# Kernel optimization log

Measured on AMD Instinct MI355X. Metric: run time of the kernel, lower is better.

The kernel has to match this reference:

```python
import jax, jax.numpy as jnp
import numpy as np

B, CIN, COUT, H, W = 8, 64, 128, 256, 256
BH = BW = 8          # block size
BC = 32              # block count per spatial dim
EPS = 1e-5


def _conv(x, w, b, pad):
    y = jax.lax.conv_general_dilated(
        x, w, (1, 1), [(pad, pad), (pad, pad)],
        dimension_numbers=("NCHW", "OIHW", "NCHW"))
    return y + b[None, :, None, None]


def _bn(x, g, b):
    # training-mode BatchNorm2d: per-channel batch stats over (N,H,W), biased var
    m = jnp.mean(x, axis=(0, 2, 3), keepdims=True)
    v = jnp.var(x, axis=(0, 2, 3), keepdims=True)
    return g[None, :, None, None] * (x - m) * jax.lax.rsqrt(v + EPS) + b[None, :, None, None]


def setup_inputs() -> dict:
    key = jax.random.key(0)
    ks = jax.random.split(key, 6)
    x = jax.random.normal(ks[0], (B, CIN, H, W), jnp.float32)
    ids = np.arange(0, B * BC * BC, 2)
    n = ids // (BC * BC)
    rem = ids % (BC * BC)
    abi = jnp.asarray(np.stack([n, rem // BC, rem % BC], axis=1), jnp.int32)

    def w(k, shape):
        return jax.random.normal(k, shape, jnp.float32) * 0.05

    C2 = 2 * COUT
    return dict(
        x=x, activeBlockIndices=abi,
        w_c=w(ks[1], (COUT, CIN, 1, 1)), b_c=jnp.zeros((COUT,), jnp.float32),
        g_c=jnp.ones((COUT,), jnp.float32), be_c=jnp.zeros((COUT,), jnp.float32),
        w1=w(ks[2], (C2, COUT, 1, 1)), b1=jnp.zeros((C2,), jnp.float32),
        g1=jnp.ones((C2,), jnp.float32), be1=jnp.zeros((C2,), jnp.float32),
        w2=w(ks[3], (C2, C2, 3, 3)), b2=jnp.zeros((C2,), jnp.float32),
        g2=jnp.ones((C2,), jnp.float32), be2=jnp.zeros((C2,), jnp.float32),
        w3=w(ks[4], (COUT, C2, 1, 1)), b3=jnp.zeros((COUT,), jnp.float32),
        g3=jnp.ones((COUT,), jnp.float32), be3=jnp.zeros((COUT,), jnp.float32),
    )


def reference(x, activeBlockIndices,
              w_c, b_c, g_c, be_c,
              w1, b1, g1, be1,
              w2, b2, g2, be2,
              w3, b3, g3, be3):
    # channel stack: 1x1 conv -> ReLU -> BN
    x = _bn(jax.nn.relu(_conv(x, w_c, b_c, 0)), g_c, be_c)  # [B, COUT, H, W]

    n = activeBlockIndices[:, 0]
    rows = activeBlockIndices[:, 1][:, None] * BH + jnp.arange(BH)  # [NB, BH]
    cols = activeBlockIndices[:, 2][:, None] * BW + jnp.arange(BW)  # [NB, BW]

    # sparse_gather: advanced indexing -> [NB, BH, BW, COUT]
    g = x[n[:, None, None], :, rows[:, :, None], cols[:, None, :]]
    g = g.transpose(0, 3, 1, 2)  # [NB, COUT, BH, BW]

    # dense stack on gathered blocks
    g = _bn(jax.nn.relu(_conv(g, w1, b1, 0)), g1, be1)
    g = _bn(jax.nn.relu(_conv(g, w2, b2, 1)), g2, be2)
    g = _bn(jax.nn.relu(_conv(g, w3, b3, 0)), g3, be3)  # [NB, COUT, BH, BW]

    # sparse_scatter back into x
    x = x.at[n[:, None, None], :, rows[:, :, None], cols[:, None, :]].set(
        g.transpose(0, 2, 3, 1))
    return x
```

## Files before the change

### kernel.cpp

```cpp
#include <hip/hip_runtime.h>
#include <hip/hip_bf16.h>
#include <stdint.h>

typedef unsigned short u16;

#define B_    8
#define CIN_  64
#define COUT_ 128
#define C2_   256
#define H_    256
#define W_    256
#define HW_   (H_*W_)
#define EPS_  1e-5f

typedef __attribute__((ext_vector_type(8))) short bf16x8;
typedef __attribute__((ext_vector_type(4))) float f32x4;

__device__ __align__(16) u16  g_R0[67108864];
__device__ __align__(16) u16  g_R1[67108864];
__device__ float g_wTa[8192];
__device__ float g_stat[4096];
__device__ __align__(16) u16 g_w2pk[1179648];
__device__ float g_S2[2304];
__device__ float g_bias2p[16384];
__device__ __align__(16) u16 g_w1pk[65536];
__device__ float g_bias1p[256];
__device__ __align__(16) u16 g_w3pk[65536];
__device__ float g_bias3p[128];

#define S_SUMA 0
#define S_SSA  128
#define S_SUM1 256
#define S_SS1  512
#define S_SUM2 768
#define S_SS2  1024
#define S_SUM3 1280
#define S_SS3  1408
#define S_SCA  1536
#define S_SHA  1664
#define S_SC1  1792
#define S_SH1  2048
#define S_SC2  2304
#define S_SH2  2560
#define S_SC3  2816
#define S_SH3  2944

__device__ __forceinline__ float u2f(u16 u){
    unsigned int x = ((unsigned int)u) << 16; float f; __builtin_memcpy(&f, &x, 4); return f;
}
__device__ __forceinline__ u16 f2u(float f){
    __hip_bfloat16 h = __float2bfloat16(f); u16 u; __builtin_memcpy(&u, &h, 2); return u;
}
__device__ __forceinline__ float bitsf(unsigned int x){ float f; __builtin_memcpy(&f, &x, 4); return f; }

__global__ void k_zero(){
    int i = blockIdx.x*blockDim.x + threadIdx.x;
    if (i < 4096) g_stat[i] = 0.f;
}

__global__ void k_prep_weights(const float* __restrict__ w_c){
    int i = blockIdx.x*blockDim.x + threadIdx.x;
    if (i < 8192){ int ci = i >> 7, co = i & 127; g_wTa[i] = w_c[co*64 + ci]; }
}

__global__ __launch_bounds__(256) void k_convA(const float* __restrict__ x,
                                               const float* __restrict__ bias){
    __shared__ float sIn[64*64];
    int tile = blockIdx.x;
    int n   = tile >> 10;
    int hw0 = (tile & 1023) << 6;
    for (int s = threadIdx.x; s < 64*64; s += 256){
        int ci = s >> 6, px = s & 63;
        sIn[s] = x[(size_t)(n*CIN_ + ci)*HW_ + hw0 + px];
    }
    __syncthreads();
    int lane = threadIdx.x & 63;
    int wv   = __builtin_amdgcn_readfirstlane(threadIdx.x >> 6);
    int co_base = blockIdx.y*64 + wv*16;
    float acc[16];
    #pragma unroll
    for (int k = 0; k < 16; k++) acc[k] = 0.f;
    for (int ci = 0; ci < 64; ci++){
        float xv = sIn[ci*64 + lane];
        const float* wrow = g_wTa + ci*COUT_ + co_base;
        #pragma unroll
        for (int k = 0; k < 16; k++) acc[k] = fmaf(xv, wrow[k], acc[k]);
    }
    #pragma unroll
    for (int k = 0; k < 16; k++){
        int co = co_base + k;
        float v = fmaxf(acc[k] + bias[co], 0.f);
        g_R0[(size_t)(n*COUT_ + co)*HW_ + hw0 + lane] = f2u(v);
    }
}

__global__ __launch_bounds__(256) void k_stats(int which, int NOuter, int C, int S, int slices,
                                               int sumOff, int ssOff){
    const u16* buf = which ? g_R1 : g_R0;
    int c  = blockIdx.x / slices;
    int sl = blockIdx.x % slices;
    int nCnt = (NOuter - sl + slices - 1) / slices;
    int S8 = S >> 3;
    long long per8 = (long long)nCnt * S8;
    float s0 = 0.f, s1 = 0.f;
    for (long long j = threadIdx.x; j < per8; j += 256){
        int nloc = (int)(j / S8);
        int s8   = (int)(j % S8);
        int n    = sl + nloc*slices;
        uint4 v = *(const uint4*)(buf + ((size_t)n*C + c)*S + s8*8);
        #pragma unroll
        for (int q = 0; q < 4; q++){
            unsigned u = (&v.x)[q];
            float a = bitsf(u << 16);
            float b = bitsf(u & 0xffff0000u);
            s0 += a + b; s1 += a*a + b*b;
        }
    }
    __shared__ float r0[256], r1[256];
    r0[threadIdx.x] = s0; r1[threadIdx.x] = s1;
    __syncthreads();
    for (int off = 128; off > 0; off >>= 1){
        if ((int)threadIdx.x < off){
            r0[threadIdx.x] += r0[threadIdx.x + off];
            r1[threadIdx.x] += r1[threadIdx.x + off];
        }
        __syncthreads();
    }
    if (threadIdx.x == 0){
        atomicAdd(&g_stat[sumOff + c], r0[0]);
        atomicAdd(&g_stat[ssOff  + c], r1[0]);
    }
}

__global__ void k_params(int sumOff, int ssOff, int scOff, int shOff,
                         const float* __restrict__ gamma, const float* __restrict__ beta,
                         float invN, int C){
    int c = blockIdx.x*blockDim.x + threadIdx.x;
    if (c >= C) return;
    float m   = g_stat[sumOff + c]*invN;
    float var = fmaxf(g_stat[ssOff + c]*invN - m*m, 0.f);
    float sc  = gamma[c] / sqrtf(var + EPS_);
    g_stat[scOff + c] = sc;
    g_stat[shOff + c] = beta[c] - m*sc;
}

__global__ __launch_bounds__(256) void k_apply_bn(float* __restrict__ out){
    size_t i8 = ((size_t)blockIdx.x*256 + threadIdx.x)*8;
    int c = (int)((i8 >> 16) & 127);
    float sc = g_stat[S_SCA + c], sh = g_stat[S_SHA + c];
    uint4 v = *(const uint4*)(g_R0 + i8);
    float4 o0, o1;
    o0.x = sc*bitsf(v.x << 16)       + sh;
    o0.y = sc*bitsf(v.x & 0xffff0000u) + sh;
    o0.z = sc*bitsf(v.y << 16)       + sh;
    o0.w = sc*bitsf(v.y & 0xffff0000u) + sh;
    o1.x = sc*bitsf(v.z << 16)       + sh;
    o1.y = sc*bitsf(v.z & 0xffff0000u) + sh;
    o1.z = sc*bitsf(v.w << 16)       + sh;
    o1.w = sc*bitsf(v.w & 0xffff0000u) + sh;
    *(float4*)(out + i8)     = o0;
    *(float4*)(out + i8 + 4) = o1;
}

__global__ __launch_bounds__(256) void k_prep_w1p(const float* __restrict__ w1){
    int id = blockIdx.x*256 + threadIdx.x;
    if (id >= 32768) return;
    int co = id & 255, ci = id >> 8;
    float wv = w1[co*128 + ci] * g_stat[S_SCA + ci];
    u16 hi = f2u(wv);
    u16 lo = f2u(wv - u2f(hi));
    int ks = ci >> 5, kin = ci & 31;
    int lanew = (kin >> 3)*16 + (co & 15);
    int j = kin & 7, ntg = co >> 4;
    size_t i0 = ((size_t)(ks*32 + ntg)*64 + lanew)*8 + j;
    g_w1pk[i0]        = hi;
    g_w1pk[i0 + 8192] = lo;
}
__global__ void k_prep_b1(const float* __restrict__ w1, const float* __restrict__ b1){
    int co = blockIdx.x;
    int ci = threadIdx.x;
    __shared__ float r[128];
    r[ci] = w1[co*128 + ci] * g_stat[S_SHA + ci];
    __syncthreads();
    for (int off = 64; off > 0; off >>= 1){
        if (ci < off) r[ci] += r[ci + off];
        __syncthreads();
    }
    if (ci == 0) g_bias1p[co] = b1[co] + r[0];
}

__global__ __launch_bounds__(256) void k_conv1m(const int* __restrict__ abi){
    __shared__ __align__(1024) u16 sA[8192];
    char* sB = (char*)sA;
    int b = blockIdx.x;
    int n = abi[b*3+0], by = abi[b*3+1], bx = abi[b*3+2];
    const u16* src = g_R0 + (size_t)n*COUT_*HW_ + (size_t)(by*8)*W_ + bx*8;
    for (int q = threadIdx.x; q < 512; q += 256){
        int ci0 = (q >> 4)*4;
        int rc  = q & 15;
        int r = rc >> 1, c0 = (rc & 1)*4;
        ushort4 v0 = *(const ushort4*)(src + (size_t)(ci0+0)*HW_ + r*W_ + c0);
        ushort4 v1 = *(const ushort4*)(src + (size_t)(ci0+1)*HW_ + r*W_ + c0);
        ushort4 v2 = *(const ushort4*)(src + (size_t)(ci0+2)*HW_ + r*W_ + c0);
        ushort4 v3 = *(const ushort4*)(src + (size_t)(ci0+3)*HW_ + r*W_ + c0);
        #pragma unroll
        for (int i = 0; i < 4; i++){
            int px  = r*8 + c0 + i;
            int off = (px*256 + ci0*2) ^ ((px & 7) << 4);
            ushort4 w;
            w.x = (&v0.x)[i]; w.y = (&v1.x)[i]; w.z = (&v2.x)[i]; w.w = (&v3.x)[i];
            *(ushort4*)(sB + off) = w;
        }
    }
    __syncthreads();
    int lane = threadIdx.x & 63;
    int wv   = __builtin_amdgcn_readfirstlane(threadIdx.x >> 6);
    int l15  = lane & 15, lg = lane >> 4;
    f32x4 acc[4][4];
    #pragma unroll
    for (int m0 = 0; m0 < 4; m0++)
        #pragma unroll
        for (int nt = 0; nt < 4; nt++) acc[m0][nt] = (f32x4){0.f,0.f,0.f,0.f};
    #pragma unroll
    for (int ks = 0; ks < 4; ks++){
        bf16x8 bh[4], bl[4];
        #pragma unroll
        for (int nt = 0; nt < 4; nt++){
            int ntg = wv*4 + nt;
            const u16* bp = g_w1pk + ((size_t)(ks*32 + ntg)*64 + lane)*8;
            bh[nt] = *(const bf16x8*)bp;
            bl[nt] = *(const bf16x8*)(bp + 8192);
        }
        bf16x8 af[4];
        #pragma unroll
        for (int m0 = 0; m0 < 4; m0++){
            int px  = m0*16 + l15;
            int off = (px*256 + ks*64 + lg*16) ^ ((px & 7) << 4);
            af[m0]  = *(const bf16x8*)(sB + off);
        }
        #pragma unroll
        for (int m0 = 0; m0 < 4; m0++)
            #pragma unroll
            for (int nt = 0; nt < 4; nt++){
                acc[m0][nt] = __builtin_amdgcn_mfma_f32_16x16x32_bf16(af[m0], bh[nt], acc[m0][nt], 0, 0, 0);
                acc[m0][nt] = __builtin_amdgcn_mfma_f32_16x16x32_bf16(af[m0], bl[nt], acc[m0][nt], 0, 0, 0);
            }
    }
    u16* dst = g_R1 + (size_t)b*C2_*64;
    #pragma unroll
    for (int m0 = 0; m0 < 4; m0++){
        int px0 = m0*16 + lg*4;
        #pragma unroll
        for (int nt = 0; nt < 4; nt++){
            int co = wv*64 + nt*16 + l15;
            float bb = g_bias1p[co];
            float f0 = fmaxf(acc[m0][nt][0] + bb, 0.f);
            float f1 = fmaxf(acc[m0][nt][1] + bb, 0.f);
            float f2 = fmaxf(acc[m0][nt][2] + bb, 0.f);
            float f3 = fmaxf(acc[m0][nt][3] + bb, 0.f);
            uint2 o;
            o.x = (unsigned)f2u(f0) | ((unsigned)f2u(f1) << 16);
            o.y = (unsigned)f2u(f2) | ((unsigned)f2u(f3) << 16);
            *(uint2*)(dst + (size_t)co*64 + px0) = o;
        }
    }
}

__global__ __launch_bounds__(256) void k_prep_w2(const float* __restrict__ w2){
    int id = blockIdx.x*256 + threadIdx.x;
    if (id >= 589824) return;
    int co  = id & 255;
    int k   = id >> 8;
    int tap = k >> 8;
    int ci  = k & 255;
    float wv = w2[((size_t)co*256 + ci)*9 + tap] * g_stat[S_SC1 + ci];
    u16 hi = f2u(wv);
    u16 lo = f2u(wv - u2f(hi));
    int ks72  = k >> 5;
    int kin   = k & 31;
    int lanew = (kin >> 3)*16 + (co & 15);
    int j     = kin & 7;
    int ntg   = co >> 4;
    size_t i0 = ((size_t)(ks72*32 + ntg)*64 + lanew)*8 + j;
    g_w2pk[i0]        = hi;
    g_w2pk[i0 + 8192] = lo;
}

__global__ __launch_bounds__(256) void k_prep_S2(const float* __restrict__ w2){
    int tc  = blockIdx.x;
    int tap = tc >> 8, co = tc & 255;
    int ci  = threadIdx.x;
    float v = w2[((size_t)co*256 + ci)*9 + tap] * g_stat[S_SH1 + ci];
    __shared__ float r[256];
    r[ci] = v; __syncthreads();
    for (int off = 128; off > 0; off >>= 1){
        if (ci < off) r[ci] += r[ci + off];
        __syncthreads();
    }
    if (ci == 0) g_S2[tc] = r[0];
}

__global__ void k_prep_bias2(const float* __restrict__ b2){
    int px = blockIdx.x;
    int co = threadIdx.x;
    int rr = px >> 3, cc = px & 7;
    float s = b2[co];
    for (int tap = 0; tap < 9; tap++){
        int dr = tap/3, dc = tap - 3*(tap/3);
        int r2 = rr + dr, c2 = cc + dc;
        if (r2 >= 1 && r2 <= 8 && c2 >= 1 && c2 <= 8) s += g_S2[tap*256 + co];
    }
    g_bias2p[px*256 + co] = s;
}

__global__ __launch_bounds__(512, 2) void k_conv2m(int NB){
    __shared__ __align__(1024) u16 sA2[51200];
    int half = threadIdx.x >> 8;
    int tid  = threadIdx.x & 255;
    int b = blockIdx.x*2 + half;
    if (b >= NB) b = NB - 1;
    char* sB = (char*)sA2 + half*51200;

    for (int s = tid; s < 36*32; s += 256){
        int cell = s >> 5, seg = s & 31;
        int L;
        if      (cell < 10) L = cell;
        else if (cell < 20) L = 90 + (cell - 10);
        else if (cell < 28) L = (cell - 19)*10;
        else                L = (cell - 27)*10 + 9;
        int off = (L*512 + seg*16) ^ ((L & 7) << 4);
        uint4 z = {0u,0u,0u,0u};
        *(uint4*)(sB + off) = z;
    }
    const u16* src = g_R1 + (size_t)b*C2_*64;
    for (int q = tid; q < 1024; q += 256){
        int px0 = (q & 15)*4;
        int ci0 = (q >> 4)*4;
        ushort4 v0 = *(const ushort4*)(src + (ci0+0)*64 + px0);
        ushort4 v1 = *(const ushort4*)(src + (ci0+1)*64 + px0);
        ushort4 v2 = *(const ushort4*)(src + (ci0+2)*64 + px0);
        ushort4 v3 = *(const ushort4*)(src + (ci0+3)*64 + px0);
        #pragma unroll
        for (int i = 0; i < 4; i++){
            int px = px0 + i;
            int L  = ((px >> 3) + 1)*10 + (px & 7) + 1;
            int off = (L*512 + ci0*2) ^ ((L & 7) << 4);
            ushort4 w;
            w.x = (&v0.x)[i]; w.y = (&v1.x)[i]; w.z = (&v2.x)[i]; w.w = (&v3.x)[i];
            *(ushort4*)(sB + off) = w;
        }
    }
    __syncthreads();

    int lane = threadIdx.x & 63;
    int wv   = __builtin_amdgcn_readfirstlane((threadIdx.x >> 6) & 3);
    int l15  = lane & 15;
    int lg   = lane >> 4;
    int rA   = l15 >> 3;
    int cA   = l15 & 7;

    f32x4 acc[4][4];
    #pragma unroll
    for (int m0 = 0; m0 < 4; m0++)
        #pragma unroll
        for (int nt = 0; nt < 4; nt++)
            acc[m0][nt] = (f32x4){0.f,0.f,0.f,0.f};

    for (int tap = 0; tap < 9; tap++){
        int dr = tap/3, dc = tap - 3*(tap/3);
        #pragma unroll
        for (int ks = 0; ks < 8; ks++){
            int ks72 = tap*8 + ks;
            const u16* bp = g_w2pk + (size_t)(ks72*32)*512;
            bf16x8 bh[4], bl[4];
            #pragma unroll
            for (int nt = 0; nt < 4; nt++){
                int ntg = wv*4 + nt;
                bh[nt] = *(const bf16x8*)(bp + ((size_t)ntg*64 + lane)*8);
                bl[nt] = *(const bf16x8*)(bp + ((size_t)(16 + ntg)*64 + lane)*8);
            }
            bf16x8 af[4];
            #pragma unroll
            for (int m0 = 0; m0 < 4; m0++){
                int L   = (m0*2 + rA + dr)*10 + cA + dc;
                int off = (L*512 + ks*64 + lg*16) ^ ((L & 7) << 4);
                af[m0]  = *(const bf16x8*)(sB + off);
            }
            #pragma unroll
            for (int m0 = 0; m0 < 4; m0++){
                #pragma unroll
                for (int nt = 0; nt < 4; nt++){
                    acc[m0][nt] = __builtin_amdgcn_mfma_f32_16x16x32_bf16(af[m0], bh[nt], acc[m0][nt], 0, 0, 0);
                    acc[m0][nt] = __builtin_amdgcn_mfma_f32_16x16x32_bf16(af[m0], bl[nt], acc[m0][nt], 0, 0, 0);
                }
            }
        }
    }

    u16* dst = g_R0 + (size_t)b*C2_*64;
    #pragma unroll
    for (int m0 = 0; m0 < 4; m0++){
        int px0 = m0*16 + lg*4;
        #pragma unroll
        for (int nt = 0; nt < 4; nt++){
            int co = wv*64 + nt*16 + l15;
            float f0 = fmaxf(acc[m0][nt][0] + g_bias2p[(px0+0)*256 + co], 0.f);
            float f1 = fmaxf(acc[m0][nt][1] + g_bias2p[(px0+1)*256 + co], 0.f);
            float f2 = fmaxf(acc[m0][nt][2] + g_bias2p[(px0+2)*256 + co], 0.f);
            float f3 = fmaxf(acc[m0][nt][3] + g_bias2p[(px0+3)*256 + co], 0.f);
            uint2 o;
            o.x = (unsigned)f2u(f0) | ((unsigned)f2u(f1) << 16);
            o.y = (unsigned)f2u(f2) | ((unsigned)f2u(f3) << 16);
            *(uint2*)(dst + (size_t)co*64 + px0) = o;
        }
    }
}

__global__ __launch_bounds__(256) void k_prep_w3p(const float* __restrict__ w3){
    int id = blockIdx.x*256 + threadIdx.x;
    if (id >= 32768) return;
    int co = id & 127, ci = id >> 7;
    float wv = w3[co*256 + ci] * g_stat[S_SC2 + ci];
    u16 hi = f2u(wv);
    u16 lo = f2u(wv - u2f(hi));
    int ks = ci >> 5, kin = ci & 31;
    int lanew = (kin >> 3)*16 + (co & 15);
    int j = kin & 7, ntg = co >> 4;
    size_t i0 = ((size_t)(ks*16 + ntg)*64 + lanew)*8 + j;
    g_w3pk[i0]        = hi;
    g_w3pk[i0 + 4096] = lo;
}
__global__ void k_prep_b3(const float* __restrict__ w3, const float* __restrict__ b3){
    int co = blockIdx.x;
    int ci = threadIdx.x;
    __shared__ float r[256];
    r[ci] = w3[co*256 + ci] * g_stat[S_SH2 + ci];
    __syncthreads();
    for (int off = 128; off > 0; off >>= 1){
        if (ci < off) r[ci] += r[ci + off];
        __syncthreads();
    }
    if (ci == 0) g_bias3p[co] = b3[co] + r[0];
}

__global__ __launch_bounds__(256) void k_conv3m(){
    __shared__ __align__(1024) u16 sA[16384];
    char* sB = (char*)sA;
    int b = blockIdx.x;
    const u16* src = g_R0 + (size_t)b*C2_*64;
    for (int q = threadIdx.x; q < 1024; q += 256){
        int px0 = (q & 15)*4;
        int ci0 = (q >> 4)*4;
        ushort4 v0 = *(const ushort4*)(src + (ci0+0)*64 + px0);
        ushort4 v1 = *(const ushort4*)(src + (ci0+1)*64 + px0);
        ushort4 v2 = *(const ushort4*)(src + (ci0+2)*64 + px0);
        ushort4 v3 = *(const ushort4*)(src + (ci0+3)*64 + px0);
        #pragma unroll
        for (int i = 0; i < 4; i++){
            int px = px0 + i;
            int off = (px*512 + ci0*2) ^ ((px & 7) << 4);
            ushort4 w;
            w.x = (&v0.x)[i]; w.y = (&v1.x)[i]; w.z = (&v2.x)[i]; w.w = (&v3.x)[i];
            *(ushort4*)(sB + off) = w;
        }
    }
    __syncthreads();
    int lane = threadIdx.x & 63;
    int wv   = __builtin_amdgcn_readfirstlane(threadIdx.x >> 6);
    int l15  = lane & 15, lg = lane >> 4;
    f32x4 acc[4][2];
    #pragma unroll
    for (int m0 = 0; m0 < 4; m0++){ acc[m0][0] = (f32x4){0.f,0.f,0.f,0.f}; acc[m0][1] = (f32x4){0.f,0.f,0.f,0.f}; }
    #pragma unroll
    for (int ks = 0; ks < 8; ks++){
        bf16x8 bh[2], bl[2];
        #pragma unroll
        for (int nt = 0; nt < 2; nt++){
            int ntg = wv*2 + nt;
            const u16* bp = g_w3pk + ((size_t)(ks*16 + ntg)*64 + lane)*8;
            bh[nt] = *(const bf16x8*)bp;
            bl[nt] = *(const bf16x8*)(bp + 4096);
        }
        bf16x8 af[4];
        #pragma unroll
        for (int m0 = 0; m0 < 4; m0++){
            int px  = m0*16 + l15;
            int off = (px*512 + ks*64 + lg*16) ^ ((px & 7) << 4);
            af[m0]  = *(const bf16x8*)(sB + off);
        }
        #pragma unroll
        for (int m0 = 0; m0 < 4; m0++)
            #pragma unroll
            for (int nt = 0; nt < 2; nt++){
                acc[m0][nt] = __builtin_amdgcn_mfma_f32_16x16x32_bf16(af[m0], bh[nt], acc[m0][nt], 0, 0, 0);
                acc[m0][nt] = __builtin_amdgcn_mfma_f32_16x16x32_bf16(af[m0], bl[nt], acc[m0][nt], 0, 0, 0);
            }
    }
    u16* dst = g_R1 + (size_t)b*COUT_*64;
    #pragma unroll
    for (int m0 = 0; m0 < 4; m0++){
        int px0 = m0*16 + lg*4;
        #pragma unroll
        for (int nt = 0; nt < 2; nt++){
            int co = wv*32 + nt*16 + l15;
            float bb = g_bias3p[co];
            float f0 = fmaxf(acc[m0][nt][0] + bb, 0.f);
            float f1 = fmaxf(acc[m0][nt][1] + bb, 0.f);
            float f2 = fmaxf(acc[m0][nt][2] + bb, 0.f);
            float f3 = fmaxf(acc[m0][nt][3] + bb, 0.f);
            uint2 o;
            o.x = (unsigned)f2u(f0) | ((unsigned)f2u(f1) << 16);
            o.y = (unsigned)f2u(f2) | ((unsigned)f2u(f3) << 16);
            *(uint2*)(dst + (size_t)co*64 + px0) = o;
        }
    }
}

__global__ __launch_bounds__(256) void k_scatter(const int* __restrict__ abi,
                                                 float* __restrict__ out){
    int b  = blockIdx.x;
    int n  = abi[b*3+0], by = abi[b*3+1], bx = abi[b*3+2];
    float* base = out + (size_t)n*COUT_*HW_ + (size_t)(by*8)*W_ + bx*8;
    const u16* src = g_R1 + (size_t)b*COUT_*64;
    for (int t = threadIdx.x; t < 1024; t += 256){
        int co = t >> 3;
        int r  = t & 7;
        float sc = g_stat[S_SC3 + co], sh = g_stat[S_SH3 + co];
        uint4 v = *(const uint4*)(src + co*64 + r*8);
        float4 o0, o1;
        o0.x = sc*bitsf(v.x << 16)         + sh;
        o0.y = sc*bitsf(v.x & 0xffff0000u) + sh;
        o0.z = sc*bitsf(v.y << 16)         + sh;
        o0.w = sc*bitsf(v.y & 0xffff0000u) + sh;
        o1.x = sc*bitsf(v.z << 16)         + sh;
        o1.y = sc*bitsf(v.z & 0xffff0000u) + sh;
        o1.z = sc*bitsf(v.w << 16)         + sh;
        o1.w = sc*bitsf(v.w & 0xffff0000u) + sh;
        float* dst = base + (size_t)co*HW_ + r*W_;
        *(float4*)dst       = o0;
        *(float4*)(dst + 4) = o1;
    }
}

extern "C" void kernel_launch(void* const* d_in, const int* in_sizes, int n_in,
                              void* d_out, int out_size, void* d_ws, size_t ws_size,
                              hipStream_t stream){
    const float* x    = (const float*)d_in[0];
    const int*   abi  = (const int*)  d_in[1];
    const float* w_c  = (const float*)d_in[2];
    const float* b_c  = (const float*)d_in[3];
    const float* ga_c = (const float*)d_in[4];
    const float* be_c = (const float*)d_in[5];
    const float* w1   = (const float*)d_in[6];
    const float* b1   = (const float*)d_in[7];
    const float* ga1  = (const float*)d_in[8];
    const float* be1  = (const float*)d_in[9];
    const float* w2   = (const float*)d_in[10];
    const float* b2   = (const float*)d_in[11];
    const float* ga2  = (const float*)d_in[12];
    const float* be2  = (const float*)d_in[13];
    const float* w3   = (const float*)d_in[14];
    const float* b3   = (const float*)d_in[15];
    const float* ga3  = (const float*)d_in[16];
    const float* be3  = (const float*)d_in[17];
    int NB = in_sizes[1] / 3;
    (void)d_ws; (void)ws_size; (void)n_in; (void)out_size;

    k_zero<<<16, 256, 0, stream>>>();
    k_prep_weights<<<32, 256, 0, stream>>>(w_c);

    k_convA<<<dim3(8192, 2), 256, 0, stream>>>(x, b_c);
    k_stats<<<128*8, 256, 0, stream>>>(0, 8, 128, 65536, 8, S_SUMA, S_SSA);
    k_params<<<1, 128, 0, stream>>>(S_SUMA, S_SSA, S_SCA, S_SHA, ga_c, be_c, 1.f/(8.f*65536.f), 128);
    k_apply_bn<<<32768, 256, 0, stream>>>((float*)d_out);

    k_prep_w1p<<<128, 256, 0, stream>>>(w1);
    k_prep_b1<<<256, 128, 0, stream>>>(w1, b1);
    k_conv1m<<<NB, 256, 0, stream>>>(abi);
    k_stats<<<256*32, 256, 0, stream>>>(1, NB, 256, 64, 32, S_SUM1, S_SS1);
    k_params<<<1, 256, 0, stream>>>(S_SUM1, S_SS1, S_SC1, S_SH1, ga1, be1, 1.f/((float)NB*64.f), 256);

    k_prep_w2<<<2304, 256, 0, stream>>>(w2);
    k_prep_S2<<<2304, 256, 0, stream>>>(w2);
    k_prep_bias2<<<64, 256, 0, stream>>>(b2);

    k_conv2m<<<(NB + 1)/2, 512, 0, stream>>>(NB);
    k_stats<<<256*32, 256, 0, stream>>>(0, NB, 256, 64, 32, S_SUM2, S_SS2);
    k_params<<<1, 256, 0, stream>>>(S_SUM2, S_SS2, S_SC2, S_SH2, ga2, be2, 1.f/((float)NB*64.f), 256);

    k_prep_w3p<<<128, 256, 0, stream>>>(w3);
    k_prep_b3<<<128, 256, 0, stream>>>(w3, b3);
    k_conv3m<<<NB, 256, 0, stream>>>();
    k_stats<<<128*32, 256, 0, stream>>>(1, NB, 128, 64, 32, S_SUM3, S_SS3);
    k_params<<<1, 128, 0, stream>>>(S_SUM3, S_SS3, S_SC3, S_SH3, ga3, be3, 1.f/((float)NB*64.f), 128);

    k_scatter<<<NB, 256, 0, stream>>>(abi, (float*)d_out);
}
```

Baseline: 1.478 ms.

## Fuse BN stats into convs, move convA to MFMA, skip active blocks in apply

Batch-norm sum and sum-of-squares accumulation now happens inside each conv epilogue. Partials go to shared memory, then to 32 striped global banks that k_params reduces, so the separate k_stats passes over the intermediates are removed. The first 1x1 conv is rewritten from scalar FMA to split-bf16 MFMA (hi/lo, three products). conv2 switches from 16x16x32 to 32x32x16 MFMA with a new weight packing. A block mask lets k_apply_bn skip writing blocks that the scatter will overwrite anyway, which saves output bandwidth at the cost of one extra mask lookup per thread.

```diff
diff --git a/kernel.cpp b/kernel.cpp
--- a/kernel.cpp
+++ b/kernel.cpp
@@ -13,12 +13,12 @@
 #define HW_   (H_*W_)
 #define EPS_  1e-5f
 
-typedef __attribute__((ext_vector_type(8))) short bf16x8;
-typedef __attribute__((ext_vector_type(4))) float f32x4;
+typedef __attribute__((ext_vector_type(8)))  short bf16x8;
+typedef __attribute__((ext_vector_type(4)))  float f32x4;
+typedef __attribute__((ext_vector_type(16))) float f32x16;
 
 __device__ __align__(16) u16  g_R0[67108864];
 __device__ __align__(16) u16  g_R1[67108864];
-__device__ float g_wTa[8192];
 __device__ float g_stat[4096];
 __device__ __align__(16) u16 g_w2pk[1179648];
 __device__ float g_S2[2304];
@@ -27,15 +27,15 @@
 __device__ float g_bias1p[256];
 __device__ __align__(16) u16 g_w3pk[65536];
 __device__ float g_bias3p[128];
-
-#define S_SUMA 0
-#define S_SSA  128
-#define S_SUM1 256
-#define S_SS1  512
-#define S_SUM2 768
-#define S_SS2  1024
-#define S_SUM3 1280
-#define S_SS3  1408
+__device__ __align__(16) u16 g_wApk[16384];
+__device__ float g_bank[65536];
+__device__ __align__(4) unsigned char g_mask[8192];
+
+#define BK_A 0
+#define BK_1 16384
+#define BK_2 32768
+#define BK_3 49152
+
 #define S_SCA  1536
 #define S_SHA  1664
 #define S_SC1  1792
@@ -55,90 +55,141 @@
 
 __global__ void k_zero(){
     int i = blockIdx.x*blockDim.x + threadIdx.x;
-    if (i < 4096) g_stat[i] = 0.f;
-}
-
-__global__ void k_prep_weights(const float* __restrict__ w_c){
-    int i = blockIdx.x*blockDim.x + threadIdx.x;
-    if (i < 8192){ int ci = i >> 7, co = i & 127; g_wTa[i] = w_c[co*64 + ci]; }
-}
-
-__global__ __launch_bounds__(256) void k_convA(const float* __restrict__ x,
-                                               const float* __restrict__ bias){
-    __shared__ float sIn[64*64];
+    g_bank[i] = 0.f;
+    if (i < 2048) ((int*)g_mask)[i] = 0;
+}
+
+__global__ void k_buildmask(const int* __restrict__ abi, int NB){
+    int b = blockIdx.x*256 + threadIdx.x;
+    if (b < NB) g_mask[abi[b*3]*1024 + abi[b*3+1]*32 + abi[b*3+2]] = 1;
+}
+
+__global__ void k_prep_wA(const float* __restrict__ w_c){
+    int id = blockIdx.x*256 + threadIdx.x;
+    if (id >= 8192) return;
+    int co = id & 127, ci = id >> 7;
+    float wv = w_c[co*64 + ci];
+    u16 hi = f2u(wv);
+    u16 lo = f2u(wv - u2f(hi));
+    int ks = ci >> 5, kin = ci & 31;
+    int lanew = (kin >> 3)*16 + (co & 15);
+    int j = kin & 7, ntg = co >> 4;
+    size_t i0 = ((size_t)(ks*8 + ntg)*64 + lanew)*8 + j;
+    g_wApk[i0]        = hi;
+    g_wApk[i0 + 8192] = lo;
+}
+
+__global__ __launch_bounds__(256) void k_convAm(const float* __restrict__ x,
+                                                const float* __restrict__ bias){
+    __shared__ __align__(1024) u16 sA[64*128];
+    __shared__ float sStat[512];
+    char* sB = (char*)sA;
     int tile = blockIdx.x;
     int n   = tile >> 10;
     int hw0 = (tile & 1023) << 6;
-    for (int s = threadIdx.x; s < 64*64; s += 256){
-        int ci = s >> 6, px = s & 63;
-        sIn[s] = x[(size_t)(n*CIN_ + ci)*HW_ + hw0 + px];
-    }
-    __syncthreads();
+    for (int t = threadIdx.x; t < 512; t += 256) sStat[t] = 0.f;
+
+    const float* xb = x + (size_t)n*CIN_*HW_ + hw0;
+    {
+        int q   = threadIdx.x;
+        int ci0 = (q >> 4)*4;
+        int px0 = (q & 15)*4;
+        float4 v0 = *(const float4*)(xb + (size_t)(ci0+0)*HW_ + px0);
+        float4 v1 = *(const float4*)(xb + (size_t)(ci0+1)*HW_ + px0);
+        float4 v2 = *(const float4*)(xb + (size_t)(ci0+2)*HW_ + px0);
+        float4 v3 = *(const float4*)(xb + (size_t)(ci0+3)*HW_ + px0);
+        #pragma unroll
+        for (int i = 0; i < 4; i++){
+            int px = px0 + i;
+            float f0 = (&v0.x)[i], f1 = (&v1.x)[i], f2 = (&v2.x)[i], f3 = (&v3.x)[i];
+            u16 h0 = f2u(f0), h1 = f2u(f1), h2 = f2u(f2), h3 = f2u(f3);
+            ushort4 hv = { h0, h1, h2, h3 };
+            ushort4 lv = { f2u(f0 - u2f(h0)), f2u(f1 - u2f(h1)),
+                           f2u(f2 - u2f(h2)), f2u(f3 - u2f(h3)) };
+            int off = (px*256 + ci0*2) ^ ((px & 7) << 4);
+            *(ushort4*)(sB + off)       = hv;
+            *(ushort4*)(sB + off + 128) = lv;
+        }
+    }
+    __syncthreads();
+
     int lane = threadIdx.x & 63;
     int wv   = __builtin_amdgcn_readfirstlane(threadIdx.x >> 6);
-    int co_base = blockIdx.y*64 + wv*16;
-    float acc[16];
-    #pragma unroll
-    for (int k = 0; k < 16; k++) acc[k] = 0.f;
-    for (int ci = 0; ci < 64; ci++){
-        float xv = sIn[ci*64 + lane];
-        const float* wrow = g_wTa + ci*COUT_ + co_base;
-        #pragma unroll
-        for (int k = 0; k < 16; k++) acc[k] = fmaf(xv, wrow[k], acc[k]);
-    }
-    #pragma unroll
-    for (int k = 0; k < 16; k++){
-        int co = co_base + k;
-        float v = fmaxf(acc[k] + bias[co], 0.f);
-        g_R0[(size_t)(n*COUT_ + co)*HW_ + hw0 + lane] = f2u(v);
-    }
-}
-
-__global__ __launch_bounds__(256) void k_stats(int which, int NOuter, int C, int S, int slices,
-                                               int sumOff, int ssOff){
-    const u16* buf = which ? g_R1 : g_R0;
-    int c  = blockIdx.x / slices;
-    int sl = blockIdx.x % slices;
-    int nCnt = (NOuter - sl + slices - 1) / slices;
-    int S8 = S >> 3;
-    long long per8 = (long long)nCnt * S8;
-    float s0 = 0.f, s1 = 0.f;
-    for (long long j = threadIdx.x; j < per8; j += 256){
-        int nloc = (int)(j / S8);
-        int s8   = (int)(j % S8);
-        int n    = sl + nloc*slices;
-        uint4 v = *(const uint4*)(buf + ((size_t)n*C + c)*S + s8*8);
-        #pragma unroll
-        for (int q = 0; q < 4; q++){
-            unsigned u = (&v.x)[q];
-            float a = bitsf(u << 16);
-            float b = bitsf(u & 0xffff0000u);
-            s0 += a + b; s1 += a*a + b*b;
-        }
-    }
-    __shared__ float r0[256], r1[256];
-    r0[threadIdx.x] = s0; r1[threadIdx.x] = s1;
-    __syncthreads();
-    for (int off = 128; off > 0; off >>= 1){
-        if ((int)threadIdx.x < off){
-            r0[threadIdx.x] += r0[threadIdx.x + off];
-            r1[threadIdx.x] += r1[threadIdx.x + off];
-        }
-        __syncthreads();
-    }
-    if (threadIdx.x == 0){
-        atomicAdd(&g_stat[sumOff + c], r0[0]);
-        atomicAdd(&g_stat[ssOff  + c], r1[0]);
-    }
-}
-
-__global__ void k_params(int sumOff, int ssOff, int scOff, int shOff,
+    int l15  = lane & 15, lg = lane >> 4;
+    f32x4 acc[4][2];
+    #pragma unroll
+    for (int m0 = 0; m0 < 4; m0++){ acc[m0][0] = (f32x4){0,0,0,0}; acc[m0][1] = (f32x4){0,0,0,0}; }
+
+    #pragma unroll
+    for (int ks = 0; ks < 2; ks++){
+        bf16x8 bh[2], bl[2];
+        #pragma unroll
+        for (int nt = 0; nt < 2; nt++){
+            int ntg = wv*2 + nt;
+            const u16* bp = g_wApk + ((size_t)(ks*8 + ntg)*64 + lane)*8;
+            bh[nt] = *(const bf16x8*)bp;
+            bl[nt] = *(const bf16x8*)(bp + 8192);
+        }
+        bf16x8 ah[4], al[4];
+        #pragma unroll
+        for (int m0 = 0; m0 < 4; m0++){
+            int px  = m0*16 + l15;
+            int off = (px*256 + ks*64 + lg*16) ^ ((px & 7) << 4);
+            ah[m0] = *(const bf16x8*)(sB + off);
+            al[m0] = *(const bf16x8*)(sB + off + 128);
+        }
+        #pragma unroll
+        for (int m0 = 0; m0 < 4; m0++)
+            #pragma unroll
+            for (int nt = 0; nt < 2; nt++){
+                acc[m0][nt] = __builtin_amdgcn_mfma_f32_16x16x32_bf16(ah[m0], bh[nt], acc[m0][nt], 0, 0, 0);
+                acc[m0][nt] = __builtin_amdgcn_mfma_f32_16x16x32_bf16(ah[m0], bl[nt], acc[m0][nt], 0, 0, 0);
+                acc[m0][nt] = __builtin_amdgcn_mfma_f32_16x16x32_bf16(al[m0], bh[nt], acc[m0][nt], 0, 0, 0);
+            }
+    }
+
+    u16* dst = g_R0 + (size_t)n*COUT_*HW_ + hw0;
+    #pragma unroll
+    for (int nt = 0; nt < 2; nt++){
+        int co = wv*32 + nt*16 + l15;
+        float bb = bias[co];
+        float s0 = 0.f, s1 = 0.f;
+        #pragma unroll
+        for (int m0 = 0; m0 < 4; m0++){
+            int px0 = m0*16 + lg*4;
+            u16 uu[4];
+            #pragma unroll
+            for (int i = 0; i < 4; i++){
+                float v = fmaxf(acc[m0][nt][i] + bb, 0.f);
+                uu[i] = f2u(v);
+                float a = u2f(uu[i]);
+                s0 += a; s1 += a*a;
+            }
+            uint2 o;
+            o.x = (unsigned)uu[0] | ((unsigned)uu[1] << 16);
+            o.y = (unsigned)uu[2] | ((unsigned)uu[3] << 16);
+            *(uint2*)(dst + (size_t)co*HW_ + px0) = o;
+        }
+        atomicAdd(&sStat[co], s0);
+        atomicAdd(&sStat[256 + co], s1);
+    }
+    __syncthreads();
+    for (int t = threadIdx.x; t < 512; t += 256)
+        atomicAdd(&g_bank[BK_A + (tile & 31)*512 + t], sStat[t]);
+}
+
+__global__ void k_params(int bkOff, int scOff, int shOff,
                          const float* __restrict__ gamma, const float* __restrict__ beta,
                          float invN, int C){
     int c = blockIdx.x*blockDim.x + threadIdx.x;
     if (c >= C) return;
-    float m   = g_stat[sumOff + c]*invN;
-    float var = fmaxf(g_stat[ssOff + c]*invN - m*m, 0.f);
+    float s0 = 0.f, s1 = 0.f;
+    for (int s = 0; s < 32; s++){
+        s0 += g_bank[bkOff + s*512 + c];
+        s1 += g_bank[bkOff + s*512 + 256 + c];
+    }
+    float m   = s0*invN;
+    float var = fmaxf(s1*invN - m*m, 0.f);
     float sc  = gamma[c] / sqrtf(var + EPS_);
     g_stat[scOff + c] = sc;
     g_stat[shOff + c] = beta[c] - m*sc;
@@ -146,17 +197,20 @@
 
 __global__ __launch_bounds__(256) void k_apply_bn(float* __restrict__ out){
     size_t i8 = ((size_t)blockIdx.x*256 + threadIdx.x)*8;
+    int hw = (int)(i8 & 65535);
+    int n  = (int)(i8 >> 23);
+    if (g_mask[(n << 10) | ((hw >> 11) << 5) | ((hw & 255) >> 3)]) return;
     int c = (int)((i8 >> 16) & 127);
     float sc = g_stat[S_SCA + c], sh = g_stat[S_SHA + c];
     uint4 v = *(const uint4*)(g_R0 + i8);
     float4 o0, o1;
-    o0.x = sc*bitsf(v.x << 16)       + sh;
+    o0.x = sc*bitsf(v.x << 16)         + sh;
     o0.y = sc*bitsf(v.x & 0xffff0000u) + sh;
-    o0.z = sc*bitsf(v.y << 16)       + sh;
+    o0.z = sc*bitsf(v.y << 16)         + sh;
     o0.w = sc*bitsf(v.y & 0xffff0000u) + sh;
-    o1.x = sc*bitsf(v.z << 16)       + sh;
+    o1.x = sc*bitsf(v.z << 16)         + sh;
     o1.y = sc*bitsf(v.z & 0xffff0000u) + sh;
-    o1.z = sc*bitsf(v.w << 16)       + sh;
+    o1.z = sc*bitsf(v.w << 16)         + sh;
     o1.w = sc*bitsf(v.w & 0xffff0000u) + sh;
     *(float4*)(out + i8)     = o0;
     *(float4*)(out + i8 + 4) = o1;
@@ -191,9 +245,11 @@
 
 __global__ __launch_bounds__(256) void k_conv1m(const int* __restrict__ abi){
     __shared__ __align__(1024) u16 sA[8192];
+    __shared__ float sStat[512];
     char* sB = (char*)sA;
     int b = blockIdx.x;
     int n = abi[b*3+0], by = abi[b*3+1], bx = abi[b*3+2];
+    for (int t = threadIdx.x; t < 512; t += 256) sStat[t] = 0.f;
     const u16* src = g_R0 + (size_t)n*COUT_*HW_ + (size_t)(by*8)*W_ + bx*8;
     for (int q = threadIdx.x; q < 512; q += 256){
         int ci0 = (q >> 4)*4;
@@ -220,7 +276,7 @@
     #pragma unroll
     for (int m0 = 0; m0 < 4; m0++)
         #pragma unroll
-        for (int nt = 0; nt < 4; nt++) acc[m0][nt] = (f32x4){0.f,0.f,0.f,0.f};
+        for (int nt = 0; nt < 4; nt++) acc[m0][nt] = (f32x4){0,0,0,0};
     #pragma unroll
     for (int ks = 0; ks < 4; ks++){
         bf16x8 bh[4], bl[4];
@@ -248,22 +304,32 @@
     }
     u16* dst = g_R1 + (size_t)b*C2_*64;
     #pragma unroll
-    for (int m0 = 0; m0 < 4; m0++){
-        int px0 = m0*16 + lg*4;
-        #pragma unroll
-        for (int nt = 0; nt < 4; nt++){
-            int co = wv*64 + nt*16 + l15;
-            float bb = g_bias1p[co];
-            float f0 = fmaxf(acc[m0][nt][0] + bb, 0.f);
-            float f1 = fmaxf(acc[m0][nt][1] + bb, 0.f);
-            float f2 = fmaxf(acc[m0][nt][2] + bb, 0.f);
-            float f3 = fmaxf(acc[m0][nt][3] + bb, 0.f);
+    for (int nt = 0; nt < 4; nt++){
+        int co = wv*64 + nt*16 + l15;
+        float bb = g_bias1p[co];
+        float s0 = 0.f, s1 = 0.f;
+        #pragma unroll
+        for (int m0 = 0; m0 < 4; m0++){
+            int px0 = m0*16 + lg*4;
+            u16 uu[4];
+            #pragma unroll
+            for (int i = 0; i < 4; i++){
+                float v = fmaxf(acc[m0][nt][i] + bb, 0.f);
+                uu[i] = f2u(v);
+                float a = u2f(uu[i]);
+                s0 += a; s1 += a*a;
+            }
             uint2 o;
-            o.x = (unsigned)f2u(f0) | ((unsigned)f2u(f1) << 16);
-            o.y = (unsigned)f2u(f2) | ((unsigned)f2u(f3) << 16);
+            o.x = (unsigned)uu[0] | ((unsigned)uu[1] << 16);
+            o.y = (unsigned)uu[2] | ((unsigned)uu[3] << 16);
             *(uint2*)(dst + (size_t)co*64 + px0) = o;
         }
-    }
+        atomicAdd(&sStat[co], s0);
+        atomicAdd(&sStat[256 + co], s1);
+    }
+    __syncthreads();
+    for (int t = threadIdx.x; t < 512; t += 256)
+        atomicAdd(&g_bank[BK_1 + (b & 31)*512 + t], sStat[t]);
 }
 
 __global__ __launch_bounds__(256) void k_prep_w2(const float* __restrict__ w2){
@@ -276,14 +342,13 @@
     float wv = w2[((size_t)co*256 + ci)*9 + tap] * g_stat[S_SC1 + ci];
     u16 hi = f2u(wv);
     u16 lo = f2u(wv - u2f(hi));
-    int ks72  = k >> 5;
-    int kin   = k & 31;
-    int lanew = (kin >> 3)*16 + (co & 15);
-    int j     = kin & 7;
-    int ntg   = co >> 4;
-    size_t i0 = ((size_t)(ks72*32 + ntg)*64 + lanew)*8 + j;
+    int ks144 = k >> 4;
+    int lanew = ((k >> 3) & 1)*32 + (co & 31);
+    int j     = k & 7;
+    int ntg   = co >> 5;
+    size_t i0 = ((size_t)(ks144*16 + ntg)*64 + lanew)*8 + j;
     g_w2pk[i0]        = hi;
-    g_w2pk[i0 + 8192] = lo;
+    g_w2pk[i0 + 4096] = lo;
 }
 
 __global__ __launch_bounds__(256) void k_prep_S2(const float* __restrict__ w2){
@@ -315,11 +380,13 @@
 
 __global__ __launch_bounds__(512, 2) void k_conv2m(int NB){
     __shared__ __align__(1024) u16 sA2[51200];
+    __shared__ float sStat[512];
     int half = threadIdx.x >> 8;
     int tid  = threadIdx.x & 255;
     int b = blockIdx.x*2 + half;
     if (b >= NB) b = NB - 1;
     char* sB = (char*)sA2 + half*51200;
+    if (threadIdx.x < 512) sStat[threadIdx.x] = 0.f;
 
     for (int s = tid; s < 36*32; s += 256){
         int cell = s >> 5, seg = s & 31;
@@ -354,66 +421,76 @@
 
     int lane = threadIdx.x & 63;
     int wv   = __builtin_amdgcn_readfirstlane((threadIdx.x >> 6) & 3);
-    int l15  = lane & 15;
-    int lg   = lane >> 4;
-    int rA   = l15 >> 3;
-    int cA   = l15 & 7;
-
-    f32x4 acc[4][4];
-    #pragma unroll
-    for (int m0 = 0; m0 < 4; m0++)
-        #pragma unroll
-        for (int nt = 0; nt < 4; nt++)
-            acc[m0][nt] = (f32x4){0.f,0.f,0.f,0.f};
+    int l31  = lane & 31;
+    int hk   = lane >> 5;
+    int pr   = l31 >> 3, pc = l31 & 7;
+    int kb   = hk*16;
+
+    f32x16 acc00 = (f32x16)(0.f), acc01 = (f32x16)(0.f);
+    f32x16 acc10 = (f32x16)(0.f), acc11 = (f32x16)(0.f);
 
     for (int tap = 0; tap < 9; tap++){
         int dr = tap/3, dc = tap - 3*(tap/3);
-        #pragma unroll
-        for (int ks = 0; ks < 8; ks++){
-            int ks72 = tap*8 + ks;
-            const u16* bp = g_w2pk + (size_t)(ks72*32)*512;
-            bf16x8 bh[4], bl[4];
+        int L0 = (pr + dr)*10 + pc + dc;
+        int L1 = L0 + 40;
+        int swz0 = (L0 & 7) << 4, swz1 = (L1 & 7) << 4;
+        int c0 = L0*512 + (kb ^ (swz0 & 16));
+        int c1 = L1*512 + (kb ^ (swz1 & 16));
+        int s056 = swz0 & 96, s156 = swz1 & 96;
+        const u16* bbase = g_w2pk + (size_t)(tap*16)*8192 + (size_t)(wv*2)*512 + (size_t)lane*8;
+        #pragma unroll
+        for (int ks = 0; ks < 16; ks++){
+            bf16x8 a0 = *(const bf16x8*)(sB + c0 + ((ks*32) ^ s056));
+            bf16x8 a1 = *(const bf16x8*)(sB + c1 + ((ks*32) ^ s156));
+            const u16* bp = bbase + (size_t)ks*8192;
+            bf16x8 bh0 = *(const bf16x8*)(bp);
+            bf16x8 bh1 = *(const bf16x8*)(bp + 512);
+            bf16x8 bl0 = *(const bf16x8*)(bp + 4096);
+            bf16x8 bl1 = *(const bf16x8*)(bp + 4608);
+            acc00 = __builtin_amdgcn_mfma_f32_32x32x16_bf16(a0, bh0, acc00, 0, 0, 0);
+            acc01 = __builtin_amdgcn_mfma_f32_32x32x16_bf16(a0, bh1, acc01, 0, 0, 0);
+            acc10 = __builtin_amdgcn_mfma_f32_32x32x16_bf16(a1, bh0, acc10, 0, 0, 0);
+            acc11 = __builtin_amdgcn_mfma_f32_32x32x16_bf16(a1, bh1, acc11, 0, 0, 0);
+            acc00 = __builtin_amdgcn_mfma_f32_32x32x16_bf16(a0, bl0, acc00, 0, 0, 0);
+            acc01 = __builtin_amdgcn_mfma_f32_32x32x16_bf16(a0, bl1, acc01, 0, 0, 0);
+            acc10 = __builtin_amdgcn_mfma_f32_32x32x16_bf16(a1, bl0, acc10, 0, 0, 0);
+            acc11 = __builtin_amdgcn_mfma_f32_32x32x16_bf16(a1, bl1, acc11, 0, 0, 0);
+        }
+    }
+
+    u16* dst = g_R0 + (size_t)b*C2_*64;
+    #pragma unroll
+    for (int nt = 0; nt < 2; nt++){
+        int co = wv*64 + nt*32 + l31;
+        float s0 = 0.f, s1 = 0.f;
+        #pragma unroll
+        for (int m0 = 0; m0 < 2; m0++){
+            const f32x16* ap = (m0 == 0) ? ((nt == 0) ? &acc00 : &acc01)
+                                         : ((nt == 0) ? &acc10 : &acc11);
             #pragma unroll
-            for (int nt = 0; nt < 4; nt++){
-                int ntg = wv*4 + nt;
-                bh[nt] = *(const bf16x8*)(bp + ((size_t)ntg*64 + lane)*8);
-                bl[nt] = *(const bf16x8*)(bp + ((size_t)(16 + ntg)*64 + lane)*8);
+            for (int q = 0; q < 4; q++){
+                int px0 = m0*32 + q*8 + hk*4;
+                const float* bp2 = g_bias2p + px0*256 + co;
+                u16 uu[4];
+                #pragma unroll
+                for (int i = 0; i < 4; i++){
+                    float v = fmaxf((*ap)[q*4 + i] + bp2[i*256], 0.f);
+                    uu[i] = f2u(v);
+                    float a = u2f(uu[i]);
+                    s0 += a; s1 += a*a;
+                }
+                uint2 o;
+                o.x = (unsigned)uu[0] | ((unsigned)uu[1] << 16);
+                o.y = (unsigned)uu[2] | ((unsigned)uu[3] << 16);
+                *(uint2*)(dst + (size_t)co*64 + px0) = o;
             }
-            bf16x8 af[4];
-            #pragma unroll
-            for (int m0 = 0; m0 < 4; m0++){
-                int L   = (m0*2 + rA + dr)*10 + cA + dc;
-                int off = (L*512 + ks*64 + lg*16) ^ ((L & 7) << 4);
-                af[m0]  = *(const bf16x8*)(sB + off);
-            }
-            #pragma unroll
-            for (int m0 = 0; m0 < 4; m0++){
-                #pragma unroll
-                for (int nt = 0; nt < 4; nt++){
-                    acc[m0][nt] = __builtin_amdgcn_mfma_f32_16x16x32_bf16(af[m0], bh[nt], acc[m0][nt], 0, 0, 0);
-                    acc[m0][nt] = __builtin_amdgcn_mfma_f32_16x16x32_bf16(af[m0], bl[nt], acc[m0][nt], 0, 0, 0);
-                }
-            }
-        }
-    }
-
-    u16* dst = g_R0 + (size_t)b*C2_*64;
-    #pragma unroll
-    for (int m0 = 0; m0 < 4; m0++){
-        int px0 = m0*16 + lg*4;
-        #pragma unroll
-        for (int nt = 0; nt < 4; nt++){
-            int co = wv*64 + nt*16 + l15;
-            float f0 = fmaxf(acc[m0][nt][0] + g_bias2p[(px0+0)*256 + co], 0.f);
-            float f1 = fmaxf(acc[m0][nt][1] + g_bias2p[(px0+1)*256 + co], 0.f);
-            float f2 = fmaxf(acc[m0][nt][2] + g_bias2p[(px0+2)*256 + co], 0.f);
-            float f3 = fmaxf(acc[m0][nt][3] + g_bias2p[(px0+3)*256 + co], 0.f);
-            uint2 o;
-            o.x = (unsigned)f2u(f0) | ((unsigned)f2u(f1) << 16);
-            o.y = (unsigned)f2u(f2) | ((unsigned)f2u(f3) << 16);
-            *(uint2*)(dst + (size_t)co*64 + px0) = o;
-        }
-    }
+        }
+        atomicAdd(&sStat[co], s0);
+        atomicAdd(&sStat[256 + co], s1);
+    }
+    __syncthreads();
+    if (threadIdx.x < 512)
+        atomicAdd(&g_bank[BK_2 + (blockIdx.x & 31)*512 + threadIdx.x], sStat[threadIdx.x]);
 }
 
 __global__ __launch_bounds__(256) void k_prep_w3p(const float* __restrict__ w3){
@@ -445,8 +522,10 @@
 
 __global__ __launch_bounds__(256) void k_conv3m(){
     __shared__ __align__(1024) u16 sA[16384];
+    __shared__ float sStat[512];
     char* sB = (char*)sA;
     int b = blockIdx.x;
+    for (int t = threadIdx.x; t < 512; t += 256) sStat[t] = 0.f;
     const u16* src = g_R0 + (size_t)b*C2_*64;
     for (int q = threadIdx.x; q < 1024; q += 256){
         int px0 = (q & 15)*4;
@@ -470,7 +549,7 @@
     int l15  = lane & 15, lg = lane >> 4;
     f32x4 acc[4][2];
     #pragma unroll
-    for (int m0 = 0; m0 < 4; m0++){ acc[m0][0] = (f32x4){0.f,0.f,0.f,0.f}; acc[m0][1] = (f32x4){0.f,0.f,0.f,0.f}; }
+    for (int m0 = 0; m0 < 4; m0++){ acc[m0][0] = (f32x4){0,0,0,0}; acc[m0][1] = (f32x4){0,0,0,0}; }
     #pragma unroll
     for (int ks = 0; ks < 8; ks++){
         bf16x8 bh[2], bl[2];
@@ -498,22 +577,32 @@
     }
     u16* dst = g_R1 + (size_t)b*COUT_*64;
     #pragma unroll
-    for (int m0 = 0; m0 < 4; m0++){
-        int px0 = m0*16 + lg*4;
-        #pragma unroll
-        for (int nt = 0; nt < 2; nt++){
-            int co = wv*32 + nt*16 + l15;
-            float bb = g_bias3p[co];
-            float f0 = fmaxf(acc[m0][nt][0] + bb, 0.f);
-            float f1 = fmaxf(acc[m0][nt][1] + bb, 0.f);
-            float f2 = fmaxf(acc[m0][nt][2] + bb, 0.f);
-            float f3 = fmaxf(acc[m0][nt][3] + bb, 0.f);
+    for (int nt = 0; nt < 2; nt++){
+        int co = wv*32 + nt*16 + l15;
+        float bb = g_bias3p[co];
+        float s0 = 0.f, s1 = 0.f;
+        #pragma unroll
+        for (int m0 = 0; m0 < 4; m0++){
+            int px0 = m0*16 + lg*4;
+            u16 uu[4];
+            #pragma unroll
+            for (int i = 0; i < 4; i++){
+                float v = fmaxf(acc[m0][nt][i] + bb, 0.f);
+                uu[i] = f2u(v);
+                float a = u2f(uu[i]);
+                s0 += a; s1 += a*a;
+            }
             uint2 o;
-            o.x = (unsigned)f2u(f0) | ((unsigned)f2u(f1) << 16);
-            o.y = (unsigned)f2u(f2) | ((unsigned)f2u(f3) << 16);
+            o.x = (unsigned)uu[0] | ((unsigned)uu[1] << 16);
+            o.y = (unsigned)uu[2] | ((unsigned)uu[3] << 16);
             *(uint2*)(dst + (size_t)co*64 + px0) = o;
         }
-    }
+        atomicAdd(&sStat[co], s0);
+        atomicAdd(&sStat[256 + co], s1);
+    }
+    __syncthreads();
+    for (int t = threadIdx.x; t < 512; t += 256)
+        atomicAdd(&g_bank[BK_3 + (b & 31)*512 + t], sStat[t]);
 }
 
 __global__ __launch_bounds__(256) void k_scatter(const int* __restrict__ abi,
@@ -566,33 +655,30 @@
     int NB = in_sizes[1] / 3;
     (void)d_ws; (void)ws_size; (void)n_in; (void)out_size;
 
-    k_zero<<<16, 256, 0, stream>>>();
-    k_prep_weights<<<32, 256, 0, stream>>>(w_c);
-
-    k_convA<<<dim3(8192, 2), 256, 0, stream>>>(x, b_c);
-    k_stats<<<128*8, 256, 0, stream>>>(0, 8, 128, 65536, 8, S_SUMA, S_SSA);
-    k_params<<<1, 128, 0, stream>>>(S_SUMA, S_SSA, S_SCA, S_SHA, ga_c, be_c, 1.f/(8.f*65536.f), 128);
+    k_zero<<<256, 256, 0, stream>>>();
+    k_prep_wA<<<32, 256, 0, stream>>>(w_c);
+    k_buildmask<<<(NB + 255)/256, 256, 0, stream>>>(abi, NB);
+
+    k_convAm<<<8192, 256, 0, stream>>>(x, b_c);
+    k_params<<<1, 128, 0, stream>>>(BK_A, S_SCA, S_SHA, ga_c, be_c, 1.f/(8.f*65536.f), 128);
     k_apply_bn<<<32768, 256, 0, stream>>>((float*)d_out);
 
     k_prep_w1p<<<128, 256, 0, stream>>>(w1);
     k_prep_b1<<<256, 128, 0, stream>>>(w1, b1);
     k_conv1m<<<NB, 256, 0, stream>>>(abi);
-    k_stats<<<256*32, 256, 0, stream>>>(1, NB, 256, 64, 32, S_SUM1, S_SS1);
-    k_params<<<1, 256, 0, stream>>>(S_SUM1, S_SS1, S_SC1, S_SH1, ga1, be1, 1.f/((float)NB*64.f), 256);
+    k_params<<<1, 256, 0, stream>>>(BK_1, S_SC1, S_SH1, ga1, be1, 1.f/((float)NB*64.f), 256);
 
     k_prep_w2<<<2304, 256, 0, stream>>>(w2);
     k_prep_S2<<<2304, 256, 0, stream>>>(w2);
     k_prep_bias2<<<64, 256, 0, stream>>>(b2);
 
     k_conv2m<<<(NB + 1)/2, 512, 0, stream>>>(NB);
-    k_stats<<<256*32, 256, 0, stream>>>(0, NB, 256, 64, 32, S_SUM2, S_SS2);
-    k_params<<<1, 256, 0, stream>>>(S_SUM2, S_SS2, S_SC2, S_SH2, ga2, be2, 1.f/((float)NB*64.f), 256);
+    k_params<<<1, 256, 0, stream>>>(BK_2, S_SC2, S_SH2, ga2, be2, 1.f/((float)NB*64.f), 256);
 
     k_prep_w3p<<<128, 256, 0, stream>>>(w3);
     k_prep_b3<<<128, 256, 0, stream>>>(w3, b3);
     k_conv3m<<<NB, 256, 0, stream>>>();
-    k_stats<<<128*32, 256, 0, stream>>>(1, NB, 128, 64, 32, S_SUM3, S_SS3);
-    k_params<<<1, 128, 0, stream>>>(S_SUM3, S_SS3, S_SC3, S_SH3, ga3, be3, 1.f/((float)NB*64.f), 128);
+    k_params<<<1, 128, 0, stream>>>(BK_3, S_SC3, S_SH3, ga3, be3, 1.f/((float)NB*64.f), 128);
 
     k_scatter<<<NB, 256, 0, stream>>>(abi, (float*)d_out);
 }
```

Result: slower. 1.779 ms (+20.3%).
